# Kernel optimization log

Hardware: AMD Instinct MI355X
Metric: run time of the kernel (lower is better)

The kernel has to match this reference:

```python
import jax, jax.numpy as jnp
import numpy as np

HIDDEN = 1024
N_HEAD = 16
HEAD_DIM = HIDDEN // N_HEAD


def setup_inputs() -> dict:
    key = jax.random.key(0)
    k1, k2, k3 = jax.random.split(key, 3)
    B, S = 4, 2048
    x = jax.random.normal(k1, (B, S, HIDDEN), dtype=jnp.float32)
    # nn.Linear(hidden, 3*hidden, bias=False): weight [3*hidden, hidden]
    w_qkv = jax.random.normal(k2, (3 * HIDDEN, HIDDEN), dtype=jnp.float32) * (HIDDEN ** -0.5)
    w_out = jax.random.normal(k3, (HIDDEN, HIDDEN), dtype=jnp.float32) * (HIDDEN ** -0.5)
    return {"x": x, "w_qkv": w_qkv, "w_out": w_out}


def _rope(q, k):
    # q, k: [B, H, S, D]
    S, D = q.shape[-2], q.shape[-1]
    pos = jnp.arange(S, dtype=jnp.float32)[:, None]          # [S, 1]
    ids = jnp.arange(D // 2, dtype=jnp.float32)              # [D/2]
    theta = jnp.power(jnp.float32(10000.0), 2.0 * ids / D)   # [D/2]
    ang = pos / theta                                        # [S, D/2]
    # torch code: sin at even slots, cos at odd slots; then repeat_interleave(2)
    sin = jnp.repeat(jnp.sin(ang), 2, axis=-1)               # [S, D]
    cos = jnp.repeat(jnp.cos(ang), 2, axis=-1)               # [S, D]

    def rot(t):
        # stack([-t_odd, t_even], -1).reshape -> interleaved rotate-half
        t2 = jnp.stack([-t[..., 1::2], t[..., 0::2]], axis=-1).reshape(t.shape)
        return t * cos + t2 * sin

    return rot(q), rot(k)


def reference(x, w_qkv, w_out):
    B, S, _ = x.shape
    qkv = jnp.einsum('bsd,ed->bse', x, w_qkv)                # [B, S, 3*hidden]
    qkv = qkv.reshape(B, S, N_HEAD, 3 * HEAD_DIM).transpose(0, 2, 1, 3)  # [B,H,S,3D]
    q, k, v = jnp.split(qkv, 3, axis=-1)                     # each [B,H,S,D]
    q, k = _rope(q, k)
    # NOTE: original forward never applies self.scale, mask (eval), or dropout.
    scores = jnp.einsum('bhqd,bhkd->bhqk', q, k)             # [B,H,S,S]
    probs = jax.nn.softmax(scores, axis=-1)
    out = jnp.einsum('bhqk,bhkd->bhqd', probs, v)            # [B,H,S,D]
    out = out.transpose(0, 2, 1, 3).reshape(B, S, HIDDEN)
    return jnp.einsum('bsd,ed->bse', out, w_out)
```

## Files before the change

### kernel.cpp

```cpp
#include <hip/hip_runtime.h>
#include <stdint.h>
#include <math.h>

#define NHEAD 16
#define HDIM 64
#define BATCH 4
#define SEQ 2048
#define NROWS (BATCH*SEQ)
#define LOG2E 1.4426950408889634f

typedef _Float16 f16x8 __attribute__((ext_vector_type(8)));
typedef _Float16 f16x4 __attribute__((ext_vector_type(4)));
typedef __fp16 h16x2 __attribute__((ext_vector_type(2)));
typedef float f32x4 __attribute__((ext_vector_type(4)));
typedef float f32x16 __attribute__((ext_vector_type(16)));
typedef unsigned int u32x4 __attribute__((ext_vector_type(4)));

typedef const __attribute__((address_space(1))) unsigned int* gas_ptr;
typedef __attribute__((address_space(3))) unsigned int* las_ptr;

__device__ __forceinline__ void gload_lds16(const void* g, void* l) {
  __builtin_amdgcn_global_load_lds((gas_ptr)g, (las_ptr)l, 16, 0, 0);
}

__device__ __forceinline__ float exp2_fast(float x) {
  float r; asm("v_exp_f32 %0, %1" : "=v"(r) : "v"(x)); return r;
}

__device__ __forceinline__ float max3f(float a, float b, float c) {
  float r; asm("v_max3_f32 %0, %1, %2, %3" : "=v"(r) : "v"(a), "v"(b), "v"(c)); return r;
}

__device__ __forceinline__ unsigned pku(float a, float b) {
  h16x2 p = __builtin_amdgcn_cvt_pkrtz(a, b);
  return __builtin_bit_cast(unsigned, p);
}

__device__ __forceinline__ float xhalf_max(float a) {
  float b;
  asm volatile("v_mov_b32 %0, %1" : "=v"(b) : "v"(a));
  asm volatile("v_permlane32_swap_b32 %0, %1" : "+v"(a), "+v"(b));
  return fmaxf(a, b);
}

__global__ void prep_kernel(const float* __restrict__ x,
                            const float* __restrict__ wq,
                            const float* __restrict__ wo,
                            unsigned short* __restrict__ xb,
                            unsigned short* __restrict__ wqb,
                            unsigned short* __restrict__ wob,
                            float2* __restrict__ tab) {
  const int idx = blockIdx.x * blockDim.x + threadIdx.x;
  const int stride = gridDim.x * blockDim.x;
  const int NS = SEQ * 32;
  const int N1 = NROWS * 1024 / 4;
  const int N2 = 3072 * 1024 / 4;
  const int N3 = 1024 * 1024 / 4;

  if (idx < NS) {
    int s = idx >> 5, j = idx & 31;
    float theta = powf(10000.0f, (float)j / 32.0f);
    float ang = (float)s / theta;
    tab[idx] = make_float2(sinf(ang), cosf(ang));
  }
  for (int i = idx; i < N1 + N2 + N3; i += stride) {
    const float* src; unsigned short* dst; int k;
    if (i < N1)            { src = x;  dst = xb;  k = i; }
    else if (i < N1 + N2)  { src = wq; dst = wqb; k = i - N1; }
    else                   { src = wo; dst = wob; k = i - N1 - N2; }
    float4 v = ((const float4*)src)[k];
    f16x4 h;
    h[0] = (_Float16)v.x; h[1] = (_Float16)v.y;
    h[2] = (_Float16)v.z; h[3] = (_Float16)v.w;
    ((f16x4*)dst)[k] = h;
  }
}

__global__ __launch_bounds__(256)
void gemm_qkv_f16(const unsigned short* __restrict__ A,
                  const unsigned short* __restrict__ B,
                  const float2* __restrict__ tab,
                  unsigned short* __restrict__ Qh,
                  unsigned short* __restrict__ Kh,
                  unsigned short* __restrict__ Vt) {
  const int K = 1024, nk = K >> 6;
  __shared__ unsigned short sA[2][128 * 64];
  __shared__ unsigned short sB[2][128 * 64];
  const int tid = threadIdx.x;
  const int lane = tid & 63;
  const int wave = tid >> 6;
  const int wr = wave >> 1, wc = wave & 1;
  const long m0 = (long)blockIdx.x * 128;
  const long n0 = (long)blockIdx.y * 128;

  f32x4 acc[4][4] = {};

  auto stage = [&](int buf, int kt) {
    const long k0 = (long)kt * 64;
    const char* Ab = (const char*)A;
    const char* Bb = (const char*)B;
#pragma unroll
    for (int qd = 0; qd < 4; ++qd) {
      int o = qd * 4096 + tid * 16;
      int row = o >> 7;
      int colb = (((o >> 4) & 7) ^ (row & 7)) << 4;
      gload_lds16(Ab + ((m0 + row) * K + k0) * 2 + colb, (char*)&sA[buf][0] + o);
      gload_lds16(Bb + ((n0 + row) * K + k0) * 2 + colb, (char*)&sB[buf][0] + o);
    }
  };

  const int lhi = lane >> 4, llo = lane & 15;
  const int rA = wr * 64 + llo;
  const int rB = wc * 64 + llo;
  int chsw[2];
#pragma unroll
  for (int s = 0; s < 2; ++s) chsw[s] = (((s * 4 + lhi) ^ (llo & 7)) << 3);

  stage(0, 0);
  __syncthreads();
  int cur = 0;

  for (int kt = 0; kt < nk; ++kt) {
    if (kt + 1 < nk) stage(cur ^ 1, kt + 1);
    f16x8 af[2][4], bfr[2][4];
#pragma unroll
    for (int s = 0; s < 2; ++s)
#pragma unroll
      for (int m = 0; m < 4; ++m)
        af[s][m] = *(const f16x8*)&sA[cur][(rA + m * 16) * 64 + chsw[s]];
#pragma unroll
    for (int s = 0; s < 2; ++s)
#pragma unroll
      for (int n = 0; n < 4; ++n)
        bfr[s][n] = *(const f16x8*)&sB[cur][(rB + n * 16) * 64 + chsw[s]];
#pragma unroll
    for (int m = 0; m < 4; ++m)
#pragma unroll
      for (int n = 0; n < 4; ++n) {
        acc[m][n] = __builtin_amdgcn_mfma_f32_16x16x32_f16(af[0][m], bfr[0][n], acc[m][n], 0, 0, 0);
        acc[m][n] = __builtin_amdgcn_mfma_f32_16x16x32_f16(af[1][m], bfr[1][n], acc[m][n], 0, 0, 0);
      }
    __syncthreads();
    cur ^= 1;
  }

  const int rb0 = (int)m0 + wr * 64 + lhi * 4;
  const int bidx = rb0 >> 11;
  const int s0 = rb0 & 2047;
#pragma unroll
  for (int n = 0; n < 4; ++n) {
    const int col = (int)n0 + wc * 64 + llo + n * 16;
    const int h = col / 192;
    const int off = col - h * 192;
    const int part = off >> 6;
    const int d = off & 63;
    const long bh_ = (long)(bidx * 16 + h);
    if (part < 2) {
      _Float16* dst = (_Float16*)(part == 0 ? Qh : Kh) + bh_ * SEQ * 64 + d;
      const float qs = (part == 0) ? LOG2E : 1.0f;
      const float2* tp = tab + (d >> 1);
      const int sgn = d & 1;
#pragma unroll
      for (int m = 0; m < 4; ++m)
#pragma unroll
        for (int r = 0; r < 4; ++r) {
          int s = s0 + m * 16 + r;
          float v = acc[m][n][r];
          float p = __shfl_xor(v, 1, 64);
          float2 sc = tp[s * 32];
          float rot = sgn ? (v * sc.y + p * sc.x) : (v * sc.y - p * sc.x);
          dst[(long)s * 64] = (_Float16)(rot * qs);
        }
    } else {
      _Float16* dst = (_Float16*)Vt + (bh_ * 64 + d) * SEQ;
#pragma unroll
      for (int m = 0; m < 4; ++m)
#pragma unroll
        for (int r = 0; r < 4; ++r)
          dst[s0 + m * 16 + r] = (_Float16)acc[m][n][r];
    }
  }
}

__global__ __launch_bounds__(512, 4)
void attn_kernel(const unsigned short* __restrict__ Qh,
                 const unsigned short* __restrict__ Kh,
                 const unsigned short* __restrict__ Vt,
                 unsigned short* __restrict__ AOut) {
  __shared__ unsigned short sK[4][64 * 64];
  __shared__ unsigned short sV[4][64 * 64];

  const int NT = SEQ / 64;
  const int tid = threadIdx.x;
  const int w = tid >> 6, lane = tid & 63;
  const int q32 = lane & 31, hi = lane >> 5;

  const int bid = blockIdx.x;
  const int xcd = bid & 7, rest = bid >> 3;
  const int bh = (rest >> 3) * 8 + xcd;
  const int qt = rest & 7;
  const int b = bh >> 4, h = bh & 15;
  const int q = qt * 256 + w * 32 + q32;

  f16x8 aq[4];
#pragma unroll
  for (int ds = 0; ds < 4; ++ds)
    aq[ds] = *(const f16x8*)&Qh[((long)bh * SEQ + q) * 64 + ds * 16 + hi * 8];

  f32x16 acc0 = {}, acc1 = {}, accl = {};
  float mrow = -INFINITY;

  const int r7 = q32 & 7;
  int off[2][4];
#pragma unroll
  for (int t = 0; t < 2; ++t)
#pragma unroll
    for (int s = 0; s < 4; ++s)
      off[t][s] = (t * 32 + q32) * 64 + (((s * 2 + hi) ^ r7) << 3);

  const int cr = tid >> 3, cp = tid & 7, cps = cp ^ (cr & 7);
  const long kSrc0 = ((long)bh * SEQ + cr) * 64 + cps * 8;
  const long vSrc0 = ((long)bh * 64 + cr) * SEQ + cps * 8;

  auto stage = [&](int buf, int kt) {
    gload_lds16(&Kh[kSrc0 + (long)kt * 4096], (char*)&sK[buf][0] + tid * 16);
    gload_lds16(&Vt[vSrc0 + (long)kt * 64],   (char*)&sV[buf][0] + tid * 16);
  };

  f16x8 vones;
#pragma unroll
  for (int j = 0; j < 8; ++j) vones[j] = (_Float16)1.0f;

#define MKPA(dst, S, R0) {                                        \
    unsigned A0 = pku(S[R0 + 0], S[R0 + 1]);                      \
    unsigned A1 = pku(S[R0 + 2], S[R0 + 3]);                      \
    unsigned B0 = pku(S[R0 + 4], S[R0 + 5]);                      \
    unsigned B1 = pku(S[R0 + 6], S[R0 + 7]);                      \
    asm("v_permlane32_swap_b32 %0, %1" : "+v"(A0), "+v"(B0));     \
    asm("v_permlane32_swap_b32 %0, %1" : "+v"(A1), "+v"(B1));     \
    u32x4 tt; tt[0] = A0; tt[1] = A1; tt[2] = B0; tt[3] = B1;     \
    dst = __builtin_bit_cast(f16x8, tt); }

  auto tile = [&](int t) {
    const unsigned short* Kb = &sK[t & 3][0];
    const unsigned short* Vb = &sV[t & 3][0];

    f32x16 s0v = {}, s1v = {};
    __builtin_amdgcn_s_setprio(1);
#pragma unroll
    for (int ds = 0; ds < 4; ++ds) {
      f16x8 k0 = *(const f16x8*)&Kb[off[0][ds]];
      f16x8 k1 = *(const f16x8*)&Kb[off[1][ds]];
      s0v = __builtin_amdgcn_mfma_f32_32x32x16_f16(k0, aq[ds], s0v, 0, 0, 0);
      s1v = __builtin_amdgcn_mfma_f32_32x32x16_f16(k1, aq[ds], s1v, 0, 0, 0);
    }
    __builtin_amdgcn_s_setprio(0);

    float t0 = max3f(s0v[0], s0v[1], s0v[2]);
    float t1 = max3f(s0v[3], s0v[4], s0v[5]);
    float t2 = max3f(s0v[6], s0v[7], s0v[8]);
    float t3 = max3f(s0v[9], s0v[10], s0v[11]);
    float t4 = max3f(s0v[12], s0v[13], s0v[14]);
    float t5 = max3f(s0v[15], s1v[0], s1v[1]);
    float t6 = max3f(s1v[2], s1v[3], s1v[4]);
    float t7 = max3f(s1v[5], s1v[6], s1v[7]);
    float t8 = max3f(s1v[8], s1v[9], s1v[10]);
    float t9 = max3f(s1v[11], s1v[12], s1v[13]);
    float t10 = fmaxf(s1v[14], s1v[15]);
    float u0 = max3f(t0, t1, t2);
    float u1 = max3f(t3, t4, t5);
    float u2 = max3f(t6, t7, t8);
    float u3 = fmaxf(t9, t10);
    float tmax = xhalf_max(fmaxf(max3f(u0, u1, u2), u3));

    if (__any(tmax > mrow + 8.0f)) {
      float mnew = fmaxf(mrow, tmax);
      float al = exp2_fast(mrow - mnew);
      mrow = mnew;
#pragma unroll
      for (int r = 0; r < 16; ++r) { acc0[r] *= al; acc1[r] *= al; accl[r] *= al; }
    }
    const float mr = mrow;

#pragma unroll
    for (int r = 0; r < 16; ++r) {
      s0v[r] = exp2_fast(s0v[r] - mr);
      s1v[r] = exp2_fast(s1v[r] - mr);
    }

    f16x8 pa[4];
    MKPA(pa[0], s0v, 0);
    MKPA(pa[1], s0v, 8);
    MKPA(pa[2], s1v, 0);
    MKPA(pa[3], s1v, 8);

    __builtin_amdgcn_s_setprio(1);
#pragma unroll
    for (int ks = 0; ks < 4; ++ks) {
      f16x8 v0 = *(const f16x8*)&Vb[off[0][ks]];
      f16x8 v1 = *(const f16x8*)&Vb[off[1][ks]];
      acc0 = __builtin_amdgcn_mfma_f32_32x32x16_f16(v0, pa[ks], acc0, 0, 0, 0);
      acc1 = __builtin_amdgcn_mfma_f32_32x32x16_f16(v1, pa[ks], acc1, 0, 0, 0);
      accl = __builtin_amdgcn_mfma_f32_32x32x16_f16(vones, pa[ks], accl, 0, 0, 0);
    }
    __builtin_amdgcn_s_setprio(0);
  };

  stage(0, 0); stage(1, 1);
  __syncthreads();

  for (int it = 0; it < NT / 2; ++it) {
    const int t0 = it * 2;
    if (it + 1 < NT / 2) { stage((t0 + 2) & 3, t0 + 2); stage((t0 + 3) & 3, t0 + 3); }
    tile(t0);
    tile(t0 + 1);
    __syncthreads();
  }

  float inv = 1.f / accl[0];
  const long obase = ((long)b * SEQ + q) * 1024 + h * 64;
#define EPI(ACCV, DT)                                              \
  {                                                                \
    _Pragma("unroll")                                              \
    for (int rg = 0; rg < 4; ++rg) {                               \
      f16x4 o;                                                     \
      _Pragma("unroll")                                            \
      for (int e = 0; e < 4; ++e)                                  \
        o[e] = (_Float16)(ACCV[rg * 4 + e] * inv);                 \
      *(f16x4*)&AOut[obase + DT * 32 + rg * 8 + hi * 4] = o;       \
    }                                                              \
  }
  EPI(acc0, 0);
  EPI(acc1, 1);
}

__global__ __launch_bounds__(256)
void gemm_out_f16(const unsigned short* __restrict__ A,
                  const unsigned short* __restrict__ B,
                  float* __restrict__ C, int M, int N, int K) {
  __shared__ unsigned short sA[2][128 * 64];
  __shared__ unsigned short sB[2][128 * 64];
  const int tid = threadIdx.x;
  const int lane = tid & 63;
  const int wave = tid >> 6;
  const int wr = wave >> 1, wc = wave & 1;
  const long m0 = (long)blockIdx.x * 128;
  const long n0 = (long)blockIdx.y * 128;

  f32x4 acc[4][4] = {};

  auto stage = [&](int buf, int kt) {
    const long k0 = (long)kt * 64;
    const char* Ab = (const char*)A;
    const char* Bb = (const char*)B;
#pragma unroll
    for (int qd = 0; qd < 4; ++qd) {
      int o = qd * 4096 + tid * 16;
      int row = o >> 7;
      int colb = (((o >> 4) & 7) ^ (row & 7)) << 4;
      gload_lds16(Ab + ((m0 + row) * K + k0) * 2 + colb, (char*)&sA[buf][0] + o);
      gload_lds16(Bb + ((n0 + row) * K + k0) * 2 + colb, (char*)&sB[buf][0] + o);
    }
  };

  const int lhi = lane >> 4, llo = lane & 15;
  const int rA = wr * 64 + llo;
  const int rB = wc * 64 + llo;
  int chsw[2];
#pragma unroll
  for (int s = 0; s < 2; ++s) chsw[s] = (((s * 4 + lhi) ^ (llo & 7)) << 3);

  const int nk = K >> 6;
  stage(0, 0);
  __syncthreads();
  int cur = 0;

  for (int kt = 0; kt < nk; ++kt) {
    if (kt + 1 < nk) stage(cur ^ 1, kt + 1);
    f16x8 af[2][4], bfr[2][4];
#pragma unroll
    for (int s = 0; s < 2; ++s)
#pragma unroll
      for (int m = 0; m < 4; ++m)
        af[s][m] = *(const f16x8*)&sA[cur][(rA + m * 16) * 64 + chsw[s]];
#pragma unroll
    for (int s = 0; s < 2; ++s)
#pragma unroll
      for (int n = 0; n < 4; ++n)
        bfr[s][n] = *(const f16x8*)&sB[cur][(rB + n * 16) * 64 + chsw[s]];
#pragma unroll
    for (int m = 0; m < 4; ++m)
#pragma unroll
      for (int n = 0; n < 4; ++n) {
        acc[m][n] = __builtin_amdgcn_mfma_f32_16x16x32_f16(af[0][m], bfr[0][n], acc[m][n], 0, 0, 0);
        acc[m][n] = __builtin_amdgcn_mfma_f32_16x16x32_f16(af[1][m], bfr[1][n], acc[m][n], 0, 0, 0);
      }
    __syncthreads();
    cur ^= 1;
  }

  const long rbase = m0 + wr * 64 + lhi * 4;
#pragma unroll
  for (int n = 0; n < 4; ++n) {
    const long col = n0 + wc * 64 + llo + n * 16;
#pragma unroll
    for (int m = 0; m < 4; ++m)
#pragma unroll
      for (int r = 0; r < 4; ++r)
        C[(rbase + m * 16 + r) * N + col] = acc[m][n][r];
  }
}

extern "C" void kernel_launch(void* const* d_in, const int* in_sizes, int n_in,
                              void* d_out, int out_size, void* d_ws, size_t ws_size,
                              hipStream_t stream) {
  const float* x     = (const float*)d_in[0];
  const float* w_qkv = (const float*)d_in[1];
  const float* w_out = (const float*)d_in[2];
  float* out = (float*)d_out;
  char* ws = (char*)d_ws;

  unsigned short* xb    = (unsigned short*)(ws + 0);
  unsigned short* attnb = xb;
  unsigned short* wqkvb = (unsigned short*)(ws + 16777216);
  unsigned short* woutb = (unsigned short*)(ws + 23068672);
  unsigned short* Qh    = (unsigned short*)(ws + 25165824);
  unsigned short* Kh    = (unsigned short*)(ws + 41943040);
  unsigned short* Vt    = (unsigned short*)(ws + 58720256);
  float2*         tab   = (float2*)(ws + 75497472);

  prep_kernel<<<2048, 256, 0, stream>>>(x, w_qkv, w_out, xb, wqkvb, woutb, tab);
  gemm_qkv_f16<<<dim3(64, 24), 256, 0, stream>>>(xb, wqkvb, tab, Qh, Kh, Vt);
  attn_kernel<<<512, 512, 0, stream>>>(Qh, Kh, Vt, attnb);
  gemm_out_f16<<<dim3(64, 8), 256, 0, stream>>>(attnb, woutb, out, NROWS, 1024, 1024);
}
```

Baseline: 200.1 us.

## Compute softmax row sums on VALU and issue both QK tiles before softmax

Drops the extra MFMA against a ones vector that built the softmax denominator. The row sum is now taken with VALU adds plus a cross-half permlane swap, in fp32 rather than from fp16-rounded probabilities. The loop also splits each tile into a QK step and a softmax+PV step, and issues both QK matmuls of the pair before their softmaxes so MFMA work can overlap the exp/VALU work. This removes a third of the PV-stage MFMAs but adds VALU adds and keeps two extra score accumulators live, which raises register pressure.

```diff
diff --git a/kernel.cpp b/kernel.cpp
--- a/kernel.cpp
+++ b/kernel.cpp
@@ -41,6 +41,12 @@
   asm volatile("v_mov_b32 %0, %1" : "=v"(b) : "v"(a));
   asm volatile("v_permlane32_swap_b32 %0, %1" : "+v"(a), "+v"(b));
   return fmaxf(a, b);
+}
+__device__ __forceinline__ float xhalf_add(float a) {
+  float b;
+  asm volatile("v_mov_b32 %0, %1" : "=v"(b) : "v"(a));
+  asm volatile("v_permlane32_swap_b32 %0, %1" : "+v"(a), "+v"(b));
+  return a + b;
 }
 
 __global__ void prep_kernel(const float* __restrict__ x,
@@ -207,8 +213,8 @@
   for (int ds = 0; ds < 4; ++ds)
     aq[ds] = *(const f16x8*)&Qh[((long)bh * SEQ + q) * 64 + ds * 16 + hi * 8];
 
-  f32x16 acc0 = {}, acc1 = {}, accl = {};
-  float mrow = -INFINITY;
+  f32x16 acc0 = {}, acc1 = {};
+  float mrow = -INFINITY, lrow = 0.f;
 
   const int r7 = q32 & 7;
   int off[2][4];
@@ -226,10 +232,6 @@
     gload_lds16(&Kh[kSrc0 + (long)kt * 4096], (char*)&sK[buf][0] + tid * 16);
     gload_lds16(&Vt[vSrc0 + (long)kt * 64],   (char*)&sV[buf][0] + tid * 16);
   };
-
-  f16x8 vones;
-#pragma unroll
-  for (int j = 0; j < 8; ++j) vones[j] = (_Float16)1.0f;
 
 #define MKPA(dst, S, R0) {                                        \
     unsigned A0 = pku(S[R0 + 0], S[R0 + 1]);                      \
@@ -241,21 +243,22 @@
     u32x4 tt; tt[0] = A0; tt[1] = A1; tt[2] = B0; tt[3] = B1;     \
     dst = __builtin_bit_cast(f16x8, tt); }
 
-  auto tile = [&](int t) {
+  auto qk = [&](int t, f32x16& z0, f32x16& z1) {
     const unsigned short* Kb = &sK[t & 3][0];
-    const unsigned short* Vb = &sV[t & 3][0];
-
-    f32x16 s0v = {}, s1v = {};
+    f32x16 a = {}, c = {};
     __builtin_amdgcn_s_setprio(1);
 #pragma unroll
     for (int ds = 0; ds < 4; ++ds) {
       f16x8 k0 = *(const f16x8*)&Kb[off[0][ds]];
       f16x8 k1 = *(const f16x8*)&Kb[off[1][ds]];
-      s0v = __builtin_amdgcn_mfma_f32_32x32x16_f16(k0, aq[ds], s0v, 0, 0, 0);
-      s1v = __builtin_amdgcn_mfma_f32_32x32x16_f16(k1, aq[ds], s1v, 0, 0, 0);
+      a = __builtin_amdgcn_mfma_f32_32x32x16_f16(k0, aq[ds], a, 0, 0, 0);
+      c = __builtin_amdgcn_mfma_f32_32x32x16_f16(k1, aq[ds], c, 0, 0, 0);
     }
     __builtin_amdgcn_s_setprio(0);
-
+    z0 = a; z1 = c;
+  };
+
+  auto smpv = [&](int t, f32x16& s0v, f32x16& s1v) {
     float t0 = max3f(s0v[0], s0v[1], s0v[2]);
     float t1 = max3f(s0v[3], s0v[4], s0v[5]);
     float t2 = max3f(s0v[6], s0v[7], s0v[8]);
@@ -278,7 +281,8 @@
       float al = exp2_fast(mrow - mnew);
       mrow = mnew;
 #pragma unroll
-      for (int r = 0; r < 16; ++r) { acc0[r] *= al; acc1[r] *= al; accl[r] *= al; }
+      for (int r = 0; r < 16; ++r) { acc0[r] *= al; acc1[r] *= al; }
+      lrow *= al;
     }
     const float mr = mrow;
 
@@ -287,6 +291,15 @@
       s0v[r] = exp2_fast(s0v[r] - mr);
       s1v[r] = exp2_fast(s1v[r] - mr);
     }
+
+    float sa[16];
+#pragma unroll
+    for (int r = 0; r < 16; ++r) sa[r] = s0v[r] + s1v[r];
+#pragma unroll
+    for (int d = 8; d > 0; d >>= 1)
+#pragma unroll
+      for (int r = 0; r < d; ++r) sa[r] = sa[r] + sa[r + d];
+    lrow += xhalf_add(sa[0]);
 
     f16x8 pa[4];
     MKPA(pa[0], s0v, 0);
@@ -294,6 +307,7 @@
     MKPA(pa[2], s1v, 0);
     MKPA(pa[3], s1v, 8);
 
+    const unsigned short* Vb = &sV[t & 3][0];
     __builtin_amdgcn_s_setprio(1);
 #pragma unroll
     for (int ks = 0; ks < 4; ++ks) {
@@ -301,7 +315,6 @@
       f16x8 v1 = *(const f16x8*)&Vb[off[1][ks]];
       acc0 = __builtin_amdgcn_mfma_f32_32x32x16_f16(v0, pa[ks], acc0, 0, 0, 0);
       acc1 = __builtin_amdgcn_mfma_f32_32x32x16_f16(v1, pa[ks], acc1, 0, 0, 0);
-      accl = __builtin_amdgcn_mfma_f32_32x32x16_f16(vones, pa[ks], accl, 0, 0, 0);
     }
     __builtin_amdgcn_s_setprio(0);
   };
@@ -312,12 +325,15 @@
   for (int it = 0; it < NT / 2; ++it) {
     const int t0 = it * 2;
     if (it + 1 < NT / 2) { stage((t0 + 2) & 3, t0 + 2); stage((t0 + 3) & 3, t0 + 3); }
-    tile(t0);
-    tile(t0 + 1);
+    f32x16 x0, x1, y0, y1;
+    qk(t0, x0, x1);
+    qk(t0 + 1, y0, y1);
+    smpv(t0, x0, x1);
+    smpv(t0 + 1, y0, y1);
     __syncthreads();
   }
 
-  float inv = 1.f / accl[0];
+  float inv = 1.f / lrow;
   const long obase = ((long)b * SEQ + q) * 1024 + h * 64;
 #define EPI(ACCV, DT)                                              \
   {                                                                \
```

After: 212.0 us. +5.9%, slower.
